# Kernel optimization log

Hardware: AMD Instinct MI355X
Metric: run time of the kernel (lower is better)

Reference implementation:

```python
import jax, jax.numpy as jnp
import numpy as np
from functools import partial

EPS = 1e-5
TAU = 0.1

def bn(x, g, b, axes):
    m = jnp.mean(x, axis=axes, keepdims=True)
    v = jnp.var(x, axis=axes, keepdims=True)
    return (x - m) * jax.lax.rsqrt(v + EPS) * g + b

def conv(x, w, b):
    # x: NCHW, w: OIHW, stride 1, padding 1
    y = jax.lax.conv_general_dilated(x, w, (1, 1), ((1, 1), (1, 1)),
                                     dimension_numbers=('NCHW', 'OIHW', 'NCHW'))
    return y + b[None, :, None, None]

def maxpool2(x):
    return jax.lax.reduce_window(x, -jnp.inf, jax.lax.max, (1, 1, 2, 2), (1, 1, 2, 2), 'VALID')

def setup_inputs() -> dict:
    key = jax.random.key(0)
    ks = jax.random.split(key, 24)
    s = 0.02
    B = 4096
    d = {}
    d['input_data'] = jax.random.normal(ks[0], (B, 3, 32, 32), jnp.float32)
    d['conv1_w'] = jax.random.normal(ks[1], (32, 3, 3, 3), jnp.float32) * s
    d['conv1_b'] = jnp.zeros((32,), jnp.float32)
    d['bn1_g'] = jnp.ones((32,), jnp.float32); d['bn1_b'] = jnp.zeros((32,), jnp.float32)
    d['conv2_w'] = jax.random.normal(ks[2], (64, 32, 3, 3), jnp.float32) * s
    d['conv2_b'] = jnp.zeros((64,), jnp.float32)
    d['bn2_g'] = jnp.ones((64,), jnp.float32); d['bn2_b'] = jnp.zeros((64,), jnp.float32)
    d['conv3_w'] = jax.random.normal(ks[3], (128, 64, 3, 3), jnp.float32) * s
    d['conv3_b'] = jnp.zeros((128,), jnp.float32)
    d['bn3_g'] = jnp.ones((128,), jnp.float32); d['bn3_b'] = jnp.zeros((128,), jnp.float32)
    d['pre_w'] = jax.random.normal(ks[4], (1024, 8192), jnp.float32) * s
    d['pre_b'] = jnp.zeros((1024,), jnp.float32)
    d['bnp_g'] = jnp.ones((1024,), jnp.float32); d['bnp_b'] = jnp.zeros((1024,), jnp.float32)
    d['disc_w'] = jax.random.normal(ks[5], (384, 1024), jnp.float32) * s
    d['disc_b'] = jnp.zeros((384,), jnp.float32)
    d['bnd_g'] = jnp.ones((384,), jnp.float32); d['bnd_b'] = jnp.zeros((384,), jnp.float32)
    d['dfc_w'] = jax.random.normal(ks[6], (2, 384), jnp.float32) * s
    d['dfc_b'] = jnp.zeros((2,), jnp.float32)
    d['sw_w'] = jax.random.normal(ks[7], (2, 384), jnp.float32) * s
    d['sw_b'] = jnp.zeros((2,), jnp.float32)
    # partitioned classifier: P=2, Linear(1024 -> 192) + ReLU + Linear(192 -> 10)
    d['p1_w'] = jax.random.normal(ks[8], (2, 192, 1024), jnp.float32) * s
    d['p1_b'] = jnp.zeros((2, 192), jnp.float32)
    d['p2_w'] = jax.random.normal(ks[9], (2, 10, 192), jnp.float32) * s
    d['p2_b'] = jnp.zeros((2, 10), jnp.float32)
    return d

def reference(input_data, conv1_w, conv1_b, bn1_g, bn1_b, conv2_w, conv2_b, bn2_g, bn2_b,
              conv3_w, conv3_b, bn3_g, bn3_b, pre_w, pre_b, bnp_g, bnp_b,
              disc_w, disc_b, bnd_g, bnd_b, dfc_w, dfc_b, sw_w, sw_b,
              p1_w, p1_b, p2_w, p2_b):
    B = input_data.shape[0]
    # feature extractor
    x = jax.nn.relu(bn(conv(input_data, conv1_w, conv1_b), bn1_g[None, :, None, None], bn1_b[None, :, None, None], (0, 2, 3)))
    x = maxpool2(x)
    x = jax.nn.relu(bn(conv(x, conv2_w, conv2_b), bn2_g[None, :, None, None], bn2_b[None, :, None, None], (0, 2, 3)))
    x = maxpool2(x)
    x = jax.nn.relu(bn(conv(x, conv3_w, conv3_b), bn3_g[None, :, None, None], bn3_b[None, :, None, None], (0, 2, 3)))
    feat = x.reshape(B, -1)  # [B, 8192]
    feat = jax.nn.relu(bn(feat @ pre_w.T + pre_b, bnp_g[None, :], bnp_b[None, :], (0,)))  # [B, 1024]
    # discriminator branch
    dpen = jax.nn.relu(bn(feat @ disc_w.T + disc_b, bnd_g[None, :], bnd_b[None, :], (0,)))  # [B, 384]
    domain_output = dpen @ dfc_w.T + dfc_b  # [B, 2]
    sw_logits = dpen @ sw_w.T + sw_b  # [B, P]
    # gumbel-softmax (soft) + multinomial sample of partition
    key = jax.random.key(42)
    k1, k2 = jax.random.split(key)
    u = jax.random.uniform(k1, sw_logits.shape, jnp.float32, 1e-10, 1.0)
    gumbel = -jnp.log(-jnp.log(u))
    y = jax.nn.softmax((sw_logits + gumbel) / TAU, axis=-1)  # [B, P]
    partition_idx = jax.random.categorical(k2, jnp.log(y + 1e-20), axis=-1)  # [B]
    # per-partition expert MLP computed densely (P=2), then gather chosen partition
    h = jax.nn.relu(jnp.einsum('bi,poi->pbo', feat, p1_w) + p1_b[:, None, :])  # [P, B, 192]
    logits = jnp.einsum('pbo,pco->pbc', h, p2_w) + p2_b[:, None, :]  # [P, B, 10]
    sel = logits[partition_idx, jnp.arange(B)]  # [B, 10]
    # original multiplies single-element stack by full gumbel vector and sums -> scale by sum(y)=1
    class_output_partitioned = sel * jnp.sum(y, axis=1, keepdims=True)
    return (class_output_partitioned, domain_output, partition_idx)
```

## Files before the change

### kernel.cpp

```cpp
#include <hip/hip_runtime.h>
#include <cstdint>
#include <cstddef>

typedef __attribute__((ext_vector_type(8))) short short8;
typedef __attribute__((ext_vector_type(4))) float f32x4;

__host__ __device__ inline void threefry2x32(uint32_t k0, uint32_t k1,
                                             uint32_t x0, uint32_t x1,
                                             uint32_t& o0, uint32_t& o1) {
  uint32_t ks2 = k0 ^ k1 ^ 0x1BD11BDAu;
  uint32_t v0 = x0 + k0, v1 = x1 + k1;
#define TF_R(r) { v0 += v1; v1 = (v1 << (r)) | (v1 >> (32 - (r))); v1 ^= v0; }
  TF_R(13) TF_R(15) TF_R(26) TF_R(6)
  v0 += k1; v1 += ks2 + 1u;
  TF_R(17) TF_R(29) TF_R(16) TF_R(24)
  v0 += ks2; v1 += k0 + 2u;
  TF_R(13) TF_R(15) TF_R(26) TF_R(6)
  v0 += k0; v1 += k1 + 3u;
  TF_R(17) TF_R(29) TF_R(16) TF_R(24)
  v0 += k1; v1 += ks2 + 4u;
  TF_R(13) TF_R(15) TF_R(26) TF_R(6)
  v0 += ks2; v1 += k0 + 5u;
#undef TF_R
  o0 = v0; o1 = v1;
}

__device__ __forceinline__ uint32_t tf_bits32(uint32_t k0, uint32_t k1, uint32_t j) {
  uint32_t o0, o1;
  threefry2x32(k0, k1, 0u, j, o0, o1);
  return o0 ^ o1;
}

__device__ __forceinline__ float u01_from_bits(uint32_t bits) {
  return __uint_as_float((bits >> 9) | 0x3f800000u) - 1.0f;
}

__device__ __forceinline__ float waveSum(float v) {
#pragma unroll
  for (int off = 32; off > 0; off >>= 1) v += __shfl_down(v, off, 64);
  return v;
}

__global__ __launch_bounds__(256) void conv1_fused_kernel(
    const float* __restrict__ in, const float* __restrict__ w,
    float* __restrict__ outraw, float* __restrict__ partials) {
  __shared__ float ins[3 * 34 * 34];
  __shared__ float red[4][64];
  const int b = blockIdx.x, t = threadIdx.x;
  for (int i = t; i < 3 * 34 * 34; i += 256) {
    int ci = i / 1156, r = i % 1156, iy = r / 34, ix = r % 34;
    int y = iy - 1, x = ix - 1;
    float v = 0.f;
    if ((unsigned)y < 32u && (unsigned)x < 32u)
      v = in[(((size_t)b * 3 + ci) * 32 + y) * 32 + x];
    ins[i] = v;
  }
  __syncthreads();
  const int py = t >> 4, px = t & 15, wv = t >> 6, ln = t & 63;
  float win[3][4][4];
#pragma unroll
  for (int ci = 0; ci < 3; ci++)
#pragma unroll
    for (int r = 0; r < 4; r++)
#pragma unroll
      for (int c = 0; c < 4; c++)
        win[ci][r][c] = ins[ci * 1156 + (2 * py + r) * 34 + (2 * px + c)];
#pragma unroll 1
  for (int co = 0; co < 32; co++) {
    float acc00 = 0.f, acc01 = 0.f, acc10 = 0.f, acc11 = 0.f;
#pragma unroll
    for (int ci = 0; ci < 3; ci++) {
      const float* wp = w + (co * 3 + ci) * 9;
#pragma unroll
      for (int dy = 0; dy < 3; dy++)
#pragma unroll
        for (int dx = 0; dx < 3; dx++) {
          float wvv = wp[dy * 3 + dx];
          acc00 += win[ci][dy][dx] * wvv;
          acc01 += win[ci][dy][dx + 1] * wvv;
          acc10 += win[ci][dy + 1][dx] * wvv;
          acc11 += win[ci][dy + 1][dx + 1] * wvv;
        }
    }
    float sm = acc00 + acc01 + acc10 + acc11;
    float sq = acc00 * acc00 + acc01 * acc01 + acc10 * acc10 + acc11 * acc11;
    float s = waveSum(sm), q = waveSum(sq);
    if (ln == 0) { red[wv][2 * co] = s; red[wv][2 * co + 1] = q; }
    float m = fmaxf(fmaxf(acc00, acc01), fmaxf(acc10, acc11));
    outraw[(((size_t)b * 32 + co) * 16 + py) * 16 + px] = m;
  }
  __syncthreads();
  for (int i = t; i < 64; i += 256)
    partials[(size_t)b * 64 + i] = red[0][i] + red[1][i] + red[2][i] + red[3][i];
}

__device__ __forceinline__ uint32_t pack_bf16q(float x) {
  uint32_t u = __float_as_uint(x);
  uint32_t hi = (u + 0x7fffu + ((u >> 16) & 1u)) & 0xffff0000u;
  float r = x - __uint_as_float(hi);
  uint32_t v = __float_as_uint(r);
  uint32_t lo = (v + 0x7fffu + ((v >> 16) & 1u)) >> 16;
  return hi | lo;
}

__global__ void cvt_bf16q_kernel(const float* X, uint32_t* Y, int n4) {
  int i = blockIdx.x * blockDim.x + threadIdx.x;
  if (i >= n4) return;
  float4 x = ((const float4*)X)[i];
  uint4 o;
  o.x = pack_bf16q(x.x); o.y = pack_bf16q(x.y);
  o.z = pack_bf16q(x.z); o.w = pack_bf16q(x.w);
  ((uint4*)Y)[i] = o;
}

__global__ void prep_w2_kernel(const float* __restrict__ w, short* __restrict__ wh,
                               short* __restrict__ wl) {
  int idx = blockIdx.x * 256 + threadIdx.x;
  if (idx >= 64 * 32 * 9) return;
  int tp = idx % 9, rem = idx / 9;
  int ci = rem % 32, co = rem / 32;
  uint32_t pq = pack_bf16q(w[idx]);
  size_t o = ((size_t)tp * 64 + co) * 32 + ci;
  wh[o] = (short)(pq >> 16);
  wl[o] = (short)(pq & 0xffffu);
}

__global__ void prep_w3_kernel(const float* __restrict__ w, short* __restrict__ wh,
                               short* __restrict__ wl) {
  int idx = blockIdx.x * 256 + threadIdx.x;
  if (idx >= 128 * 64 * 9) return;
  int tp = idx % 9, rem = idx / 9;
  int ci = rem % 64, co = rem / 64;
  uint32_t pq = pack_bf16q(w[idx]);
  size_t o = ((size_t)tp * 128 + co) * 64 + ci;
  wh[o] = (short)(pq >> 16);
  wl[o] = (short)(pq & 0xffffu);
}

__global__ __launch_bounds__(256) void conv2_mfma_kernel(
    const uint32_t* __restrict__ inq, const short* __restrict__ wh,
    const short* __restrict__ wl, float* __restrict__ outpool,
    float* __restrict__ partials) {
  __shared__ short Xh[324 * 32], Xl[324 * 32];
  __shared__ float red[4][128];
  const int b = blockIdx.x, t = threadIdx.x;
  for (int i = t; i < 324 * 16; i += 256) {
    int row = i >> 4;
    int py = row / 18, pxx = row % 18;
    if (py == 0 || py == 17 || pxx == 0 || pxx == 17) {
      ((uint32_t*)Xh)[i] = 0u;
      ((uint32_t*)Xl)[i] = 0u;
    }
  }
  for (int i = t; i < 4096; i += 256) {
    int p = i >> 8, px = i & 255;
    int y = px >> 4, x = px & 15;
    uint32_t ua = inq[((size_t)b * 32 + 2 * p) * 256 + px];
    uint32_t ub = inq[((size_t)b * 32 + 2 * p + 1) * 256 + px];
    uint32_t h = (ua >> 16) | (ub & 0xffff0000u);
    uint32_t l = (ua & 0xffffu) | (ub << 16);
    int row = (y + 1) * 18 + (x + 1);
    int ci2 = (2 * p) ^ ((row & 3) << 3);
    ((uint32_t*)Xh)[(row * 32 + ci2) >> 1] = h;
    ((uint32_t*)Xl)[(row * 32 + ci2) >> 1] = l;
  }
  __syncthreads();
  const int w = t >> 6, l = t & 63;
  const int lr = l & 15, lg = l >> 4;
  f32x4 acc[4][4];
#pragma unroll
  for (int i = 0; i < 4; i++)
#pragma unroll
    for (int j = 0; j < 4; j++) acc[i][j] = (f32x4){0.f, 0.f, 0.f, 0.f};
#pragma unroll 1
  for (int tap = 0; tap < 9; tap++) {
    const int dy = tap / 3, dx = tap % 3;
    short8 awh[4], awl[4];
#pragma unroll
    for (int i = 0; i < 4; i++) {
      size_t off = ((size_t)tap * 64 + i * 16 + lr) * 32 + lg * 8;
      awh[i] = *(const short8*)(wh + off);
      awl[i] = *(const short8*)(wl + off);
    }
    short8 bxh[4], bxl[4];
#pragma unroll
    for (int j = 0; j < 4; j++) {
      int y = w * 4 + j, x = lr;
      int row = (y + dy) * 18 + (x + dx);
      int ci = (lg * 8) ^ ((row & 3) << 3);
      bxh[j] = *(const short8*)&Xh[row * 32 + ci];
      bxl[j] = *(const short8*)&Xl[row * 32 + ci];
    }
#pragma unroll
    for (int i = 0; i < 4; i++)
#pragma unroll
      for (int j = 0; j < 4; j++) {
        acc[i][j] = __builtin_amdgcn_mfma_f32_16x16x32_bf16(awh[i], bxh[j], acc[i][j], 0, 0, 0);
        acc[i][j] = __builtin_amdgcn_mfma_f32_16x16x32_bf16(awh[i], bxl[j], acc[i][j], 0, 0, 0);
        acc[i][j] = __builtin_amdgcn_mfma_f32_16x16x32_bf16(awl[i], bxh[j], acc[i][j], 0, 0, 0);
      }
  }
#pragma unroll
  for (int i = 0; i < 4; i++)
#pragma unroll
    for (int r = 0; r < 4; r++) {
      int co = i * 16 + lg * 4 + r;
      float v0 = acc[i][0][r], v1 = acc[i][1][r], v2 = acc[i][2][r], v3 = acc[i][3][r];
      float s = v0 + v1 + v2 + v3;
      float q = v0 * v0 + v1 * v1 + v2 * v2 + v3 * v3;
#pragma unroll
      for (int off = 1; off <= 8; off <<= 1) {
        s += __shfl_xor(s, off, 64);
        q += __shfl_xor(q, off, 64);
      }
      if (lr == 0) { red[w][2 * co] = s; red[w][2 * co + 1] = q; }
      float h0 = fmaxf(v0, __shfl_xor(v0, 1, 64));
      float h1 = fmaxf(v1, __shfl_xor(v1, 1, 64));
      float h2 = fmaxf(v2, __shfl_xor(v2, 1, 64));
      float h3 = fmaxf(v3, __shfl_xor(v3, 1, 64));
      float pm0 = fmaxf(h0, h1);
      float pm1 = fmaxf(h2, h3);
      if ((lr & 1) == 0) {
        size_t base = ((size_t)b * 64 + co) * 64 + (w * 2) * 8 + (lr >> 1);
        outpool[base] = pm0;
        outpool[base + 8] = pm1;
      }
    }
  __syncthreads();
  for (int i = t; i < 128; i += 256)
    partials[(size_t)b * 128 + i] = red[0][i] + red[1][i] + red[2][i] + red[3][i];
}

__global__ __launch_bounds__(256) void conv3_mfma_kernel(
    const uint32_t* __restrict__ inq, const short* __restrict__ wh,
    const short* __restrict__ wl, float* __restrict__ outraw,
    float* __restrict__ partials) {
  __shared__ short Xh[100 * 64], Xl[100 * 64];
  __shared__ float red[256];
  const int b = blockIdx.x, t = threadIdx.x;
  for (int i = t; i < 100 * 32; i += 256) {
    int row = i >> 5;
    int py = row / 10, pxx = row % 10;
    if (py == 0 || py == 9 || pxx == 0 || pxx == 9) {
      ((uint32_t*)Xh)[i] = 0u;
      ((uint32_t*)Xl)[i] = 0u;
    }
  }
  for (int i = t; i < 2048; i += 256) {
    int p = i >> 6, px = i & 63;
    int y = px >> 3, x = px & 7;
    uint32_t ua = inq[((size_t)b * 64 + 2 * p) * 64 + px];
    uint32_t ub = inq[((size_t)b * 64 + 2 * p + 1) * 64 + px];
    uint32_t h = (ua >> 16) | (ub & 0xffff0000u);
    uint32_t l = (ua & 0xffffu) | (ub << 16);
    int row = (y + 1) * 10 + (x + 1);
    int ci2 = (2 * p) ^ ((row & 7) << 3);
    ((uint32_t*)Xh)[(row * 64 + ci2) >> 1] = h;
    ((uint32_t*)Xl)[(row * 64 + ci2) >> 1] = l;
  }
  __syncthreads();
  const int w = t >> 6, l = t & 63;
  const int lr = l & 15, lg = l >> 4;
  const int co_base = w * 32;
  f32x4 acc[2][4];
#pragma unroll
  for (int i = 0; i < 2; i++)
#pragma unroll
    for (int j = 0; j < 4; j++) acc[i][j] = (f32x4){0.f, 0.f, 0.f, 0.f};
#pragma unroll 1
  for (int tap = 0; tap < 9; tap++) {
    const int dy = tap / 3, dx = tap % 3;
#pragma unroll
    for (int sl = 0; sl < 2; sl++) {
      short8 awh[2], awl[2];
#pragma unroll
      for (int i = 0; i < 2; i++) {
        size_t off = ((size_t)tap * 128 + co_base + i * 16 + lr) * 64 + sl * 32 + lg * 8;
        awh[i] = *(const short8*)(wh + off);
        awl[i] = *(const short8*)(wl + off);
      }
      short8 bxh[4], bxl[4];
#pragma unroll
      for (int j = 0; j < 4; j++) {
        int px = j * 16 + lr;
        int row = ((px >> 3) + dy) * 10 + (px & 7) + dx;
        int ci = (sl * 32 + lg * 8) ^ ((row & 7) << 3);
        bxh[j] = *(const short8*)&Xh[row * 64 + ci];
        bxl[j] = *(const short8*)&Xl[row * 64 + ci];
      }
#pragma unroll
      for (int i = 0; i < 2; i++)
#pragma unroll
        for (int j = 0; j < 4; j++) {
          acc[i][j] = __builtin_amdgcn_mfma_f32_16x16x32_bf16(awh[i], bxh[j], acc[i][j], 0, 0, 0);
          acc[i][j] = __builtin_amdgcn_mfma_f32_16x16x32_bf16(awh[i], bxl[j], acc[i][j], 0, 0, 0);
          acc[i][j] = __builtin_amdgcn_mfma_f32_16x16x32_bf16(awl[i], bxh[j], acc[i][j], 0, 0, 0);
        }
    }
  }
#pragma unroll
  for (int i = 0; i < 2; i++)
#pragma unroll
    for (int r = 0; r < 4; r++) {
      int co = co_base + i * 16 + lg * 4 + r;
      float s = 0.f, q = 0.f;
#pragma unroll
      for (int j = 0; j < 4; j++) {
        float v = acc[i][j][r];
        outraw[((size_t)b * 128 + co) * 64 + j * 16 + lr] = v;
        s += v; q += v * v;
      }
#pragma unroll
      for (int off = 1; off <= 8; off <<= 1) {
        s += __shfl_xor(s, off, 64);
        q += __shfl_xor(q, off, 64);
      }
      if (lr == 0) { red[2 * co] = s; red[2 * co + 1] = q; }
    }
  __syncthreads();
  for (int i = t; i < 256; i += 256) partials[(size_t)b * 256 + i] = red[i];
}

__global__ __launch_bounds__(256) void reduce_partials_kernel(
    const float* __restrict__ partials, int nblk, int Q, double* __restrict__ sums) {
  int q = blockIdx.x;
  double acc = 0.0;
  for (int i = threadIdx.x; i < nblk; i += 256) acc += (double)partials[(size_t)i * Q + q];
  __shared__ double red[256];
  red[threadIdx.x] = acc;
  __syncthreads();
  for (int s = 128; s > 0; s >>= 1) {
    if (threadIdx.x < s) red[threadIdx.x] += red[threadIdx.x + s];
    __syncthreads();
  }
  if (threadIdx.x == 0) sums[q] = red[0];
}

__global__ __launch_bounds__(1024) void col_stats_kernel(
    const float* __restrict__ X, int R, int C, int nch, double* __restrict__ sums) {
  int c0 = blockIdx.x * 64, chunk = blockIdx.y;
  int cl = threadIdx.x & 63, rg = threadIdx.x >> 6;
  int rows = R / nch, rbeg = chunk * rows, rend = rbeg + rows;
  double s = 0.0, sq = 0.0;
  for (int r = rbeg + rg; r < rend; r += 16) {
    float v = X[(size_t)r * C + c0 + cl];
    s += v; sq += (double)v * (double)v;
  }
  __shared__ double red[16][64][2];
  red[rg][cl][0] = s; red[rg][cl][1] = sq;
  __syncthreads();
  if (rg == 0) {
    for (int i = 1; i < 16; i++) { s += red[i][cl][0]; sq += red[i][cl][1]; }
    sums[(size_t)chunk * 2 * C + 2 * (c0 + cl)] = s;
    sums[(size_t)chunk * 2 * C + 2 * (c0 + cl) + 1] = sq;
  }
}

__global__ void bn_finalize_kernel(const double* __restrict__ sums, int nch, int cst2,
                                   const float* __restrict__ g, const float* __restrict__ b,
                                   float* __restrict__ scale, float* __restrict__ shift,
                                   int C, double invN) {
  int c = blockIdx.x * blockDim.x + threadIdx.x;
  if (c >= C) return;
  double s = 0.0, sq = 0.0;
  for (int ch = 0; ch < nch; ch++) {
    s += sums[(size_t)ch * cst2 + 2 * c];
    sq += sums[(size_t)ch * cst2 + 2 * c + 1];
  }
  double m = s * invN;
  double v = sq * invN - m * m;
  double sc = (double)g[c] / sqrt(v + 1e-5);
  scale[c] = (float)sc;
  shift[c] = (float)((double)b[c] - m * sc);
}

template <int LOGHW, int CMASK>
__global__ void bn_relu_pack_vec4_kernel(float* __restrict__ X,
                                         const float* __restrict__ scale,
                                         const float* __restrict__ shift, int n4) {
  int i = blockIdx.x * blockDim.x + threadIdx.x;
  if (i >= n4) return;
  int c = ((i << 2) >> LOGHW) & CMASK;
  float4 v = ((float4*)X)[i];
  float sc = scale[c], sh = shift[c];
  uint4 o;
  o.x = pack_bf16q(fmaxf(v.x * sc + sh, 0.f));
  o.y = pack_bf16q(fmaxf(v.y * sc + sh, 0.f));
  o.z = pack_bf16q(fmaxf(v.z * sc + sh, 0.f));
  o.w = pack_bf16q(fmaxf(v.w * sc + sh, 0.f));
  ((uint4*)X)[i] = o;
}

__global__ void bn_relu_pack_cols4_kernel(float* __restrict__ X,
                                          const float* __restrict__ scale,
                                          const float* __restrict__ shift,
                                          int n4, int C4) {
  int i = blockIdx.x * blockDim.x + threadIdx.x;
  if (i >= n4) return;
  int c4 = i % C4;
  float4 v = ((float4*)X)[i];
  float4 sc = ((const float4*)scale)[c4];
  float4 sh = ((const float4*)shift)[c4];
  uint4 o;
  o.x = pack_bf16q(fmaxf(v.x * sc.x + sh.x, 0.f));
  o.y = pack_bf16q(fmaxf(v.y * sc.y + sh.y, 0.f));
  o.z = pack_bf16q(fmaxf(v.z * sc.z + sh.z, 0.f));
  o.w = pack_bf16q(fmaxf(v.w * sc.w + sh.w, 0.f));
  ((uint4*)X)[i] = o;
}

__global__ void bn_relu_cols4_kernel(float* __restrict__ X, const float* __restrict__ scale,
                                     const float* __restrict__ shift, int n4, int C4) {
  int i = blockIdx.x * blockDim.x + threadIdx.x;
  if (i >= n4) return;
  int c4 = i % C4;
  float4 v = ((float4*)X)[i];
  float4 sc = ((const float4*)scale)[c4];
  float4 sh = ((const float4*)shift)[c4];
  v.x = fmaxf(v.x * sc.x + sh.x, 0.f);
  v.y = fmaxf(v.y * sc.y + sh.y, 0.f);
  v.z = fmaxf(v.z * sc.z + sh.z, 0.f);
  v.w = fmaxf(v.w * sc.w + sh.w, 0.f);
  ((float4*)X)[i] = v;
}

__global__ void add_vec4_kernel(float* __restrict__ X, const float* __restrict__ Y, int n4) {
  int i = blockIdx.x * blockDim.x + threadIdx.x;
  if (i >= n4) return;
  float4 a = ((float4*)X)[i];
  float4 b = ((const float4*)Y)[i];
  a.x += b.x; a.y += b.y; a.z += b.z; a.w += b.w;
  ((float4*)X)[i] = a;
}

__device__ __forceinline__ int swz16(int row) {
  return ((row & 3) ^ ((row >> 2) & 3)) << 3;
}

template <int BIASRELU>
__global__ __launch_bounds__(256) void gemm_bf16q_kernel(
    const uint32_t* __restrict__ A, const uint32_t* __restrict__ B,
    const float* __restrict__ bias, float* __restrict__ C, int M, int N, int K) {
  __shared__ short Ah[128 * 32], Al[128 * 32], Bh[64 * 32], Bl[64 * 32];
  const int t = threadIdx.x;
  const int nTN = N >> 6;
  const int mPer = (M >> 7) >> 3;
  const int bid = blockIdx.x;
  const int xcd = bid & 7, qq = bid >> 3;
  const int m0 = (xcd * mPer + qq / nTN) << 7;
  const int n0 = (qq % nTN) << 6;
  const int w = t >> 6, l = t & 63;
  const int wrow = (w >> 1) << 6, wcol = (w & 1) << 5;
  const int lr = l & 15, lg = l >> 4;
  const int ar = t >> 1, akh = (t & 1) << 4;
  const int br = t >> 2, bkh = (t & 3) << 3;
  const int asw = swz16(ar), bsw = swz16(br);
  const uint32_t* Ap = A + (size_t)(m0 + ar) * K + akh;
  const uint32_t* Bp = B + (size_t)(n0 + br) * K + bkh;
  f32x4 acc[4][2];
#pragma unroll
  for (int i = 0; i < 4; i++)
#pragma unroll
    for (int j = 0; j < 2; j++) acc[i][j] = (f32x4){0.f, 0.f, 0.f, 0.f};
  uint4 ra0 = *(const uint4*)(Ap + 0), ra1 = *(const uint4*)(Ap + 4);
  uint4 ra2 = *(const uint4*)(Ap + 8), ra3 = *(const uint4*)(Ap + 12);
  uint4 rb0 = *(const uint4*)(Bp + 0), rb1 = *(const uint4*)(Bp + 4);
  const int NS = K >> 5;
#define STORE_G(ARR_H, ARR_L, ROW, KB, SW, U)                                   \
    {                                                                           \
      uint32_t h0 = (U.x >> 16) | (U.y & 0xffff0000u);                          \
      uint32_t h1 = (U.z >> 16) | (U.w & 0xffff0000u);                          \
      uint32_t l0 = (U.x & 0xffffu) | (U.y << 16);                              \
      uint32_t l1 = (U.z & 0xffffu) | (U.w << 16);                              \
      int idx = (ROW) * 32 + ((KB) ^ (SW));                                     \
      *(uint2*)&ARR_H[idx] = make_uint2(h0, h1);                                \
      *(uint2*)&ARR_L[idx] = make_uint2(l0, l1);                                \
    }
  for (int s = 0; s < NS; s++) {
    __syncthreads();
    STORE_G(Ah, Al, ar, akh + 0, asw, ra0)
    STORE_G(Ah, Al, ar, akh + 4, asw, ra1)
    STORE_G(Ah, Al, ar, akh + 8, asw, ra2)
    STORE_G(Ah, Al, ar, akh + 12, asw, ra3)
    STORE_G(Bh, Bl, br, bkh + 0, bsw, rb0)
    STORE_G(Bh, Bl, br, bkh + 4, bsw, rb1)
    __syncthreads();
    if (s + 1 < NS) {
      int ko = (s + 1) << 5;
      ra0 = *(const uint4*)(Ap + ko); ra1 = *(const uint4*)(Ap + ko + 4);
      ra2 = *(const uint4*)(Ap + ko + 8); ra3 = *(const uint4*)(Ap + ko + 12);
      rb0 = *(const uint4*)(Bp + ko); rb1 = *(const uint4*)(Bp + ko + 4);
    }
    short8 ahf[4], alf[4], bhf[2], blf[2];
#pragma unroll
    for (int i = 0; i < 4; i++) {
      int R = wrow + i * 16 + lr;
      int kk = (lg << 3) ^ swz16(R);
      ahf[i] = *(const short8*)&Ah[R * 32 + kk];
      alf[i] = *(const short8*)&Al[R * 32 + kk];
    }
#pragma unroll
    for (int j = 0; j < 2; j++) {
      int Cc = wcol + j * 16 + lr;
      int kk = (lg << 3) ^ swz16(Cc);
      bhf[j] = *(const short8*)&Bh[Cc * 32 + kk];
      blf[j] = *(const short8*)&Bl[Cc * 32 + kk];
    }
#pragma unroll
    for (int i = 0; i < 4; i++)
#pragma unroll
      for (int j = 0; j < 2; j++) {
        acc[i][j] = __builtin_amdgcn_mfma_f32_16x16x32_bf16(ahf[i], bhf[j], acc[i][j], 0, 0, 0);
        acc[i][j] = __builtin_amdgcn_mfma_f32_16x16x32_bf16(ahf[i], blf[j], acc[i][j], 0, 0, 0);
        acc[i][j] = __builtin_amdgcn_mfma_f32_16x16x32_bf16(alf[i], bhf[j], acc[i][j], 0, 0, 0);
      }
  }
#pragma unroll
  for (int i = 0; i < 4; i++)
#pragma unroll
    for (int j = 0; j < 2; j++) {
      int n = n0 + wcol + j * 16 + lr;
#pragma unroll
      for (int r = 0; r < 4; r++) {
        int m = m0 + wrow + i * 16 + lg * 4 + r;
        float v = acc[i][j][r];
        if (BIASRELU) v = fmaxf(v + bias[n], 0.f);
        C[(size_t)m * N + n] = v;
      }
    }
}

__global__ __launch_bounds__(256, 2) void gemm_bf16q_big_kernel(
    const uint32_t* __restrict__ A, const uint32_t* __restrict__ B,
    float* __restrict__ C0, float* __restrict__ C1, int M, int N, int K) {
  __shared__ short Ah[128 * 32], Al[128 * 32], Bh[128 * 32], Bl[128 * 32];
  const int t = threadIdx.x;
  const int nTN = N >> 7;
  const int tiles = (M >> 7) * nTN;
  const int mPer = (M >> 7) >> 3;
  const int split = blockIdx.x / tiles;
  const int bid = blockIdx.x % tiles;
  const int xcd = bid & 7, qq = bid >> 3;
  const int m0 = (xcd * mPer + qq / nTN) << 7;
  const int n0 = (qq % nTN) << 7;
  const int Kh = K >> 1;
  const int kbeg = split * Kh;
  float* Cout = split ? C1 : C0;
  const int w = t >> 6, l = t & 63;
  const int wrow = (w & 1) << 6, wcol = (w >> 1) << 6;
  const int lr = l & 15, lg = l >> 4;
  const int ar = t >> 1, akh = (t & 1) << 4;
  const int asw = swz16(ar);
  const uint32_t* Ap = A + (size_t)(m0 + ar) * K + kbeg + akh;
  const uint32_t* Bp = B + (size_t)(n0 + ar) * K + kbeg + akh;
  f32x4 acc[4][4];
#pragma unroll
  for (int i = 0; i < 4; i++)
#pragma unroll
    for (int j = 0; j < 4; j++) acc[i][j] = (f32x4){0.f, 0.f, 0.f, 0.f};
  uint4 ra0 = *(const uint4*)(Ap + 0), ra1 = *(const uint4*)(Ap + 4);
  uint4 ra2 = *(const uint4*)(Ap + 8), ra3 = *(const uint4*)(Ap + 12);
  uint4 rb0 = *(const uint4*)(Bp + 0), rb1 = *(const uint4*)(Bp + 4);
  uint4 rb2 = *(const uint4*)(Bp + 8), rb3 = *(const uint4*)(Bp + 12);
  const int NS = Kh >> 5;
  for (int s = 0; s < NS; s++) {
    __syncthreads();
    STORE_G(Ah, Al, ar, akh + 0, asw, ra0)
    STORE_G(Ah, Al, ar, akh + 4, asw, ra1)
    STORE_G(Ah, Al, ar, akh + 8, asw, ra2)
    STORE_G(Ah, Al, ar, akh + 12, asw, ra3)
    STORE_G(Bh, Bl, ar, akh + 0, asw, rb0)
    STORE_G(Bh, Bl, ar, akh + 4, asw, rb1)
    STORE_G(Bh, Bl, ar, akh + 8, asw, rb2)
    STORE_G(Bh, Bl, ar, akh + 12, asw, rb3)
    __syncthreads();
    if (s + 1 < NS) {
      int ko = (s + 1) << 5;
      ra0 = *(const uint4*)(Ap + ko); ra1 = *(const uint4*)(Ap + ko + 4);
      ra2 = *(const uint4*)(Ap + ko + 8); ra3 = *(const uint4*)(Ap + ko + 12);
      rb0 = *(const uint4*)(Bp + ko); rb1 = *(const uint4*)(Bp + ko + 4);
      rb2 = *(const uint4*)(Bp + ko + 8); rb3 = *(const uint4*)(Bp + ko + 12);
    }
    short8 ahf[4], alf[4], bhf[4], blf[4];
#pragma unroll
    for (int i = 0; i < 4; i++) {
      int R = wrow + i * 16 + lr;
      int kk = (lg << 3) ^ swz16(R);
      ahf[i] = *(const short8*)&Ah[R * 32 + kk];
      alf[i] = *(const short8*)&Al[R * 32 + kk];
    }
#pragma unroll
    for (int j = 0; j < 4; j++) {
      int Cc = wcol + j * 16 + lr;
      int kk = (lg << 3) ^ swz16(Cc);
      bhf[j] = *(const short8*)&Bh[Cc * 32 + kk];
      blf[j] = *(const short8*)&Bl[Cc * 32 + kk];
    }
#pragma unroll
    for (int i = 0; i < 4; i++)
#pragma unroll
      for (int j = 0; j < 4; j++) {
        acc[i][j] = __builtin_amdgcn_mfma_f32_16x16x32_bf16(ahf[i], bhf[j], acc[i][j], 0, 0, 0);
        acc[i][j] = __builtin_amdgcn_mfma_f32_16x16x32_bf16(ahf[i], blf[j], acc[i][j], 0, 0, 0);
        acc[i][j] = __builtin_amdgcn_mfma_f32_16x16x32_bf16(alf[i], bhf[j], acc[i][j], 0, 0, 0);
      }
  }
#undef STORE_G
#pragma unroll
  for (int i = 0; i < 4; i++)
#pragma unroll
    for (int j = 0; j < 4; j++) {
      int n = n0 + wcol + j * 16 + lr;
#pragma unroll
      for (int r = 0; r < 4; r++) {
        int m = m0 + wrow + i * 16 + lg * 4 + r;
        Cout[(size_t)m * N + n] = acc[i][j][r];
      }
    }
}

__global__ __launch_bounds__(256) void heads_kernel(
    const float* __restrict__ dpen, const float* __restrict__ dfc_w,
    const float* __restrict__ dfc_b, const float* __restrict__ sw_w,
    const float* __restrict__ sw_b, float* __restrict__ out_dom,
    float* __restrict__ swbuf) {
  int t = blockIdx.x * 256 + threadIdx.x;
  int b = t >> 2, j = t & 3;
  const float* row = dpen + (size_t)b * 384;
  const float* wr = (j < 2) ? (dfc_w + j * 384) : (sw_w + (j - 2) * 384);
  double s = 0.0;
  for (int k = 0; k < 384; k++) s += (double)row[k] * (double)wr[k];
  s += (double)((j < 2) ? dfc_b[j] : sw_b[j - 2]);
  if (j < 2) out_dom[b * 2 + j] = (float)s;
  else swbuf[b * 2 + (j - 2)] = (float)s;
}

__global__ __launch_bounds__(256) void partition_kernel(
    const float* __restrict__ swbuf, float* __restrict__ out_pid,
    int* __restrict__ pidxI, float* __restrict__ ysum,
    uint32_t k1a, uint32_t k1b, uint32_t k2a, uint32_t k2b) {
  int b = blockIdx.x * 256 + threadIdx.x;
  if (b >= 4096) return;
  uint32_t j0 = (uint32_t)(2 * b), j1 = (uint32_t)(2 * b + 1);
  float f0 = u01_from_bits(tf_bits32(k1a, k1b, j0));
  float f1 = u01_from_bits(tf_bits32(k1a, k1b, j1));
  const float MINV = 1e-10f;
  float u0 = fmaxf(MINV, f0 * (1.0f - MINV) + MINV);
  float u1 = fmaxf(MINV, f1 * (1.0f - MINV) + MINV);
  double g0 = -log(-log((double)u0));
  double g1 = -log(-log((double)u1));
  double s0 = (double)swbuf[2 * b], s1 = (double)swbuf[2 * b + 1];
  double x0 = (s0 + g0) / 0.1;
  double x1 = (s1 + g1) / 0.1;
  double mx = fmax(x0, x1);
  double e0 = exp(x0 - mx), e1 = exp(x1 - mx);
  double es = e0 + e1;
  double y0 = e0 / es, y1 = e1 / es;
  float h0 = u01_from_bits(tf_bits32(k2a, k2b, j0));
  float h1 = u01_from_bits(tf_bits32(k2a, k2b, j1));
  const float TINY = 1.17549435e-38f;
  float v0 = fmaxf(TINY, h0 * (1.0f - TINY) + TINY);
  float v1 = fmaxf(TINY, h1 * (1.0f - TINY) + TINY);
  double gg0 = -log(-log((double)v0));
  double gg1 = -log(-log((double)v1));
  double l0 = log(y0 + 1e-20) + gg0;
  double l1 = log(y1 + 1e-20) + gg1;
  int p = (l1 > l0) ? 1 : 0;
  out_pid[b] = (float)p;
  pidxI[b] = p;
  ysum[b] = (float)(y0 + y1);
}

__global__ __launch_bounds__(256) void final_kernel(
    const float* __restrict__ h, const float* __restrict__ p2w,
    const float* __restrict__ p2b, const int* __restrict__ pidxI,
    const float* __restrict__ ysum, float* __restrict__ out0) {
  int t = blockIdx.x * 256 + threadIdx.x;
  if (t >= 40960) return;
  int b = t / 10, c = t % 10;
  int p = pidxI[b];
  const float* hr = h + (size_t)b * 384 + p * 192;
  const float* wr = p2w + ((size_t)p * 10 + c) * 192;
  float s = 0.f;
  for (int o = 0; o < 192; o++) s += hr[o] * wr[o];
  s += p2b[p * 10 + c];
  out0[t] = s * ysum[b];
}

extern "C" void kernel_launch(void* const* d_in, const int* in_sizes, int n_in,
                              void* d_out, int out_size, void* d_ws, size_t ws_size,
                              hipStream_t stream) {
  const float* input   = (const float*)d_in[0];
  const float* conv1_w = (const float*)d_in[1];
  const float* bn1_g   = (const float*)d_in[3];
  const float* bn1_b   = (const float*)d_in[4];
  const float* conv2_w = (const float*)d_in[5];
  const float* bn2_g   = (const float*)d_in[7];
  const float* bn2_b   = (const float*)d_in[8];
  const float* conv3_w = (const float*)d_in[9];
  const float* bn3_g   = (const float*)d_in[11];
  const float* bn3_b   = (const float*)d_in[12];
  const float* pre_w   = (const float*)d_in[13];
  const float* bnp_g   = (const float*)d_in[15];
  const float* bnp_b   = (const float*)d_in[16];
  const float* disc_w  = (const float*)d_in[17];
  const float* bnd_g   = (const float*)d_in[19];
  const float* bnd_b   = (const float*)d_in[20];
  const float* dfc_w   = (const float*)d_in[21];
  const float* dfc_b   = (const float*)d_in[22];
  const float* sw_w    = (const float*)d_in[23];
  const float* sw_b    = (const float*)d_in[24];
  const float* p1_w    = (const float*)d_in[25];
  const float* p1_b    = (const float*)d_in[26];
  const float* p2_w    = (const float*)d_in[27];
  const float* p2_b    = (const float*)d_in[28];

  float* W = (float*)d_ws;
  float* pool1  = W + 0;
  uint32_t* pool1q = (uint32_t*)pool1;
  float* pool2  = W + 33554432;
  uint32_t* pool2q = (uint32_t*)pool2;
  float* act3   = W + 0;
  uint32_t* Acvt = (uint32_t*)(W + 0);
  uint32_t* Bcvt = (uint32_t*)(W + 33554432);
  uint32_t* discq = (uint32_t*)(W + 41943040);
  uint32_t* p1q   = (uint32_t*)(W + 42336256);
  float* csplit = W + 42729472;
  float* featp  = W + 50331648;
  uint32_t* featq = (uint32_t*)featp;
  short* wh3    = (short*)(W + 50331648);
  short* wl3    = (short*)(W + 50368512);
  short* wh2    = (short*)(W + 50405376);
  short* wl2    = (short*)(W + 50414592);
  float* dpen   = W + 54525952;
  float* hbuf   = W + 56098816;
  float* swbuf  = W + 57671680;
  float* ysum   = W + 57679872;
  int*   pidxI  = (int*)(W + 57683968);
  float* part   = W + 57688064;
  double* sums  = (double*)(W + 58736640);
  float* scale  = W + 58769408;
  float* shift  = W + 58770432;

  float* out_cls = (float*)d_out;
  float* out_dom = out_cls + 40960;
  float* out_pid = out_cls + 49152;

  uint32_t k1a, k1b, k2a, k2b;
  threefry2x32(0u, 42u, 0u, 0u, k1a, k1b);
  threefry2x32(0u, 42u, 0u, 1u, k2a, k2b);

  conv1_fused_kernel<<<dim3(4096), dim3(256), 0, stream>>>(input, conv1_w, pool1, part);
  reduce_partials_kernel<<<dim3(64), dim3(256), 0, stream>>>(part, 4096, 64, sums);
  bn_finalize_kernel<<<dim3(1), dim3(64), 0, stream>>>(sums, 1, 0, bn1_g, bn1_b, scale, shift, 32, 1.0 / (4096.0 * 1024.0));
  bn_relu_pack_vec4_kernel<8, 31><<<dim3(32768), dim3(256), 0, stream>>>(pool1, scale, shift, 8388608);

  prep_w2_kernel<<<dim3(72), dim3(256), 0, stream>>>(conv2_w, wh2, wl2);
  conv2_mfma_kernel<<<dim3(4096), dim3(256), 0, stream>>>(pool1q, wh2, wl2, pool2, part);
  reduce_partials_kernel<<<dim3(128), dim3(256), 0, stream>>>(part, 4096, 128, sums);
  bn_finalize_kernel<<<dim3(1), dim3(64), 0, stream>>>(sums, 1, 0, bn2_g, bn2_b, scale, shift, 64, 1.0 / (4096.0 * 256.0));
  bn_relu_pack_vec4_kernel<6, 63><<<dim3(16384), dim3(256), 0, stream>>>(pool2, scale, shift, 4194304);

  prep_w3_kernel<<<dim3(288), dim3(256), 0, stream>>>(conv3_w, wh3, wl3);
  conv3_mfma_kernel<<<dim3(4096), dim3(256), 0, stream>>>(pool2q, wh3, wl3, act3, part);
  reduce_partials_kernel<<<dim3(256), dim3(256), 0, stream>>>(part, 4096, 256, sums);
  bn_finalize_kernel<<<dim3(1), dim3(128), 0, stream>>>(sums, 1, 0, bn3_g, bn3_b, scale, shift, 128, 1.0 / (4096.0 * 64.0));
  bn_relu_pack_vec4_kernel<6, 127><<<dim3(32768), dim3(256), 0, stream>>>(act3, scale, shift, 8388608);

  cvt_bf16q_kernel<<<dim3(8192), dim3(256), 0, stream>>>(pre_w, Bcvt, 2097152);
  gemm_bf16q_big_kernel<<<dim3(512), dim3(256), 0, stream>>>(Acvt, Bcvt, featp, csplit, 4096, 1024, 8192);
  add_vec4_kernel<<<dim3(4096), dim3(256), 0, stream>>>(featp, csplit, 1048576);
  col_stats_kernel<<<dim3(16, 8), dim3(1024), 0, stream>>>(featp, 4096, 1024, 8, sums);
  bn_finalize_kernel<<<dim3(4), dim3(256), 0, stream>>>(sums, 8, 2048, bnp_g, bnp_b, scale, shift, 1024, 1.0 / 4096.0);
  bn_relu_pack_cols4_kernel<<<dim3(4096), dim3(256), 0, stream>>>(featp, scale, shift, 1048576, 256);

  cvt_bf16q_kernel<<<dim3(384), dim3(256), 0, stream>>>(disc_w, discq, 98304);
  cvt_bf16q_kernel<<<dim3(384), dim3(256), 0, stream>>>(p1_w, p1q, 98304);
  gemm_bf16q_kernel<0><<<dim3(192), dim3(256), 0, stream>>>(featq, discq, (const float*)nullptr, dpen, 4096, 384, 1024);
  col_stats_kernel<<<dim3(6, 8), dim3(1024), 0, stream>>>(dpen, 4096, 384, 8, sums);
  bn_finalize_kernel<<<dim3(2), dim3(256), 0, stream>>>(sums, 8, 768, bnd_g, bnd_b, scale, shift, 384, 1.0 / 4096.0);
  bn_relu_cols4_kernel<<<dim3(1536), dim3(256), 0, stream>>>(dpen, scale, shift, 393216, 96);

  heads_kernel<<<dim3(64), dim3(256), 0, stream>>>(dpen, dfc_w, dfc_b, sw_w, sw_b, out_dom, swbuf);
  partition_kernel<<<dim3(16), dim3(256), 0, stream>>>(swbuf, out_pid, pidxI, ysum, k1a, k1b, k2a, k2b);

  gemm_bf16q_kernel<1><<<dim3(192), dim3(256), 0, stream>>>(featq, p1q, p1_b, hbuf, 4096, 384, 1024);
  final_kernel<<<dim3(160), dim3(256), 0, stream>>>(hbuf, p2_w, p2_b, pidxI, ysum, out_cls);
}
```

Before: 927.6 us.

## Fuse BN+ReLU+pack into consumer conv/GEMM loads and parallelize heads

Removes the standalone BN-ReLU-pack passes after conv1, conv2 and conv3. Each consumer (conv2, conv3, the big GEMM) now reads raw fp32 activations, applies the per-channel scale/shift and ReLU, and packs to split bf16 on the fly. The split-K add kernel is folded into col_stats and the final BN pack, and the heads kernel is rewritten to use one wavefront per row with shuffle reductions. This saves several full read/write passes over large activation buffers. In exchange the GEMM and conv loads double in width (fp32 instead of packed) and the GEMM recomputes the conversion per tile.

```diff
diff --git a/kernel.cpp b/kernel.cpp
--- a/kernel.cpp
+++ b/kernel.cpp
@@ -103,6 +103,15 @@
   return hi | lo;
 }
 
+__device__ __forceinline__ uint4 pk4bn(float4 v, float sc, float sh) {
+  uint4 o;
+  o.x = pack_bf16q(fmaxf(v.x * sc + sh, 0.f));
+  o.y = pack_bf16q(fmaxf(v.y * sc + sh, 0.f));
+  o.z = pack_bf16q(fmaxf(v.z * sc + sh, 0.f));
+  o.w = pack_bf16q(fmaxf(v.w * sc + sh, 0.f));
+  return o;
+}
+
 __global__ void cvt_bf16q_kernel(const float* X, uint32_t* Y, int n4) {
   int i = blockIdx.x * blockDim.x + threadIdx.x;
   if (i >= n4) return;
@@ -138,7 +147,8 @@
 }
 
 __global__ __launch_bounds__(256) void conv2_mfma_kernel(
-    const uint32_t* __restrict__ inq, const short* __restrict__ wh,
+    const float* __restrict__ in, const float* __restrict__ scale1,
+    const float* __restrict__ shift1, const short* __restrict__ wh,
     const short* __restrict__ wl, float* __restrict__ outpool,
     float* __restrict__ partials) {
   __shared__ short Xh[324 * 32], Xl[324 * 32];
@@ -155,8 +165,11 @@
   for (int i = t; i < 4096; i += 256) {
     int p = i >> 8, px = i & 255;
     int y = px >> 4, x = px & 15;
-    uint32_t ua = inq[((size_t)b * 32 + 2 * p) * 256 + px];
-    uint32_t ub = inq[((size_t)b * 32 + 2 * p + 1) * 256 + px];
+    float va = in[((size_t)b * 32 + 2 * p) * 256 + px];
+    float vb = in[((size_t)b * 32 + 2 * p + 1) * 256 + px];
+    va = fmaxf(va * scale1[2 * p] + shift1[2 * p], 0.f);
+    vb = fmaxf(vb * scale1[2 * p + 1] + shift1[2 * p + 1], 0.f);
+    uint32_t ua = pack_bf16q(va), ub = pack_bf16q(vb);
     uint32_t h = (ua >> 16) | (ub & 0xffff0000u);
     uint32_t l = (ua & 0xffffu) | (ub << 16);
     int row = (y + 1) * 18 + (x + 1);
@@ -232,7 +245,8 @@
 }
 
 __global__ __launch_bounds__(256) void conv3_mfma_kernel(
-    const uint32_t* __restrict__ inq, const short* __restrict__ wh,
+    const float* __restrict__ in, const float* __restrict__ scale2,
+    const float* __restrict__ shift2, const short* __restrict__ wh,
     const short* __restrict__ wl, float* __restrict__ outraw,
     float* __restrict__ partials) {
   __shared__ short Xh[100 * 64], Xl[100 * 64];
@@ -249,8 +263,11 @@
   for (int i = t; i < 2048; i += 256) {
     int p = i >> 6, px = i & 63;
     int y = px >> 3, x = px & 7;
-    uint32_t ua = inq[((size_t)b * 64 + 2 * p) * 64 + px];
-    uint32_t ub = inq[((size_t)b * 64 + 2 * p + 1) * 64 + px];
+    float va = in[((size_t)b * 64 + 2 * p) * 64 + px];
+    float vb = in[((size_t)b * 64 + 2 * p + 1) * 64 + px];
+    va = fmaxf(va * scale2[2 * p] + shift2[2 * p], 0.f);
+    vb = fmaxf(vb * scale2[2 * p + 1] + shift2[2 * p + 1], 0.f);
+    uint32_t ua = pack_bf16q(va), ub = pack_bf16q(vb);
     uint32_t h = (ua >> 16) | (ub & 0xffff0000u);
     uint32_t l = (ua & 0xffffu) | (ub << 16);
     int row = (y + 1) * 10 + (x + 1);
@@ -337,13 +354,16 @@
 }
 
 __global__ __launch_bounds__(1024) void col_stats_kernel(
-    const float* __restrict__ X, int R, int C, int nch, double* __restrict__ sums) {
+    const float* __restrict__ X, const float* __restrict__ Y,
+    int R, int C, int nch, double* __restrict__ sums) {
   int c0 = blockIdx.x * 64, chunk = blockIdx.y;
   int cl = threadIdx.x & 63, rg = threadIdx.x >> 6;
   int rows = R / nch, rbeg = chunk * rows, rend = rbeg + rows;
   double s = 0.0, sq = 0.0;
   for (int r = rbeg + rg; r < rend; r += 16) {
-    float v = X[(size_t)r * C + c0 + cl];
+    size_t idx = (size_t)r * C + c0 + cl;
+    float v = X[idx];
+    if (Y) v += Y[idx];
     s += v; sq += (double)v * (double)v;
   }
   __shared__ double red[16][64][2];
@@ -374,24 +394,8 @@
   shift[c] = (float)((double)b[c] - m * sc);
 }
 
-template <int LOGHW, int CMASK>
-__global__ void bn_relu_pack_vec4_kernel(float* __restrict__ X,
-                                         const float* __restrict__ scale,
-                                         const float* __restrict__ shift, int n4) {
-  int i = blockIdx.x * blockDim.x + threadIdx.x;
-  if (i >= n4) return;
-  int c = ((i << 2) >> LOGHW) & CMASK;
-  float4 v = ((float4*)X)[i];
-  float sc = scale[c], sh = shift[c];
-  uint4 o;
-  o.x = pack_bf16q(fmaxf(v.x * sc + sh, 0.f));
-  o.y = pack_bf16q(fmaxf(v.y * sc + sh, 0.f));
-  o.z = pack_bf16q(fmaxf(v.z * sc + sh, 0.f));
-  o.w = pack_bf16q(fmaxf(v.w * sc + sh, 0.f));
-  ((uint4*)X)[i] = o;
-}
-
 __global__ void bn_relu_pack_cols4_kernel(float* __restrict__ X,
+                                          const float* __restrict__ Y,
                                           const float* __restrict__ scale,
                                           const float* __restrict__ shift,
                                           int n4, int C4) {
@@ -399,6 +403,10 @@
   if (i >= n4) return;
   int c4 = i % C4;
   float4 v = ((float4*)X)[i];
+  if (Y) {
+    float4 y = ((const float4*)Y)[i];
+    v.x += y.x; v.y += y.y; v.z += y.z; v.w += y.w;
+  }
   float4 sc = ((const float4*)scale)[c4];
   float4 sh = ((const float4*)shift)[c4];
   uint4 o;
@@ -422,15 +430,6 @@
   v.z = fmaxf(v.z * sc.z + sh.z, 0.f);
   v.w = fmaxf(v.w * sc.w + sh.w, 0.f);
   ((float4*)X)[i] = v;
-}
-
-__global__ void add_vec4_kernel(float* __restrict__ X, const float* __restrict__ Y, int n4) {
-  int i = blockIdx.x * blockDim.x + threadIdx.x;
-  if (i >= n4) return;
-  float4 a = ((float4*)X)[i];
-  float4 b = ((const float4*)Y)[i];
-  a.x += b.x; a.y += b.y; a.z += b.z; a.w += b.w;
-  ((float4*)X)[i] = a;
 }
 
 __device__ __forceinline__ int swz16(int row) {
@@ -531,7 +530,8 @@
 }
 
 __global__ __launch_bounds__(256, 2) void gemm_bf16q_big_kernel(
-    const uint32_t* __restrict__ A, const uint32_t* __restrict__ B,
+    const float* __restrict__ A, const uint32_t* __restrict__ B,
+    const float* __restrict__ scale, const float* __restrict__ shift,
     float* __restrict__ C0, float* __restrict__ C1, int M, int N, int K) {
   __shared__ short Ah[128 * 32], Al[128 * 32], Bh[128 * 32], Bl[128 * 32];
   const int t = threadIdx.x;
@@ -551,24 +551,28 @@
   const int lr = l & 15, lg = l >> 4;
   const int ar = t >> 1, akh = (t & 1) << 4;
   const int asw = swz16(ar);
-  const uint32_t* Ap = A + (size_t)(m0 + ar) * K + kbeg + akh;
+  const float* Ap = A + (size_t)(m0 + ar) * K + kbeg + akh;
   const uint32_t* Bp = B + (size_t)(n0 + ar) * K + kbeg + akh;
   f32x4 acc[4][4];
 #pragma unroll
   for (int i = 0; i < 4; i++)
 #pragma unroll
     for (int j = 0; j < 4; j++) acc[i][j] = (f32x4){0.f, 0.f, 0.f, 0.f};
-  uint4 ra0 = *(const uint4*)(Ap + 0), ra1 = *(const uint4*)(Ap + 4);
-  uint4 ra2 = *(const uint4*)(Ap + 8), ra3 = *(const uint4*)(Ap + 12);
+  float4 fa0 = *(const float4*)(Ap + 0), fa1 = *(const float4*)(Ap + 4);
+  float4 fa2 = *(const float4*)(Ap + 8), fa3 = *(const float4*)(Ap + 12);
   uint4 rb0 = *(const uint4*)(Bp + 0), rb1 = *(const uint4*)(Bp + 4);
   uint4 rb2 = *(const uint4*)(Bp + 8), rb3 = *(const uint4*)(Bp + 12);
   const int NS = Kh >> 5;
   for (int s = 0; s < NS; s++) {
+    int ch = (kbeg + akh + (s << 5)) >> 6;
+    float sc = scale[ch], sh = shift[ch];
+    uint4 ua0 = pk4bn(fa0, sc, sh), ua1 = pk4bn(fa1, sc, sh);
+    uint4 ua2 = pk4bn(fa2, sc, sh), ua3 = pk4bn(fa3, sc, sh);
     __syncthreads();
-    STORE_G(Ah, Al, ar, akh + 0, asw, ra0)
-    STORE_G(Ah, Al, ar, akh + 4, asw, ra1)
-    STORE_G(Ah, Al, ar, akh + 8, asw, ra2)
-    STORE_G(Ah, Al, ar, akh + 12, asw, ra3)
+    STORE_G(Ah, Al, ar, akh + 0, asw, ua0)
+    STORE_G(Ah, Al, ar, akh + 4, asw, ua1)
+    STORE_G(Ah, Al, ar, akh + 8, asw, ua2)
+    STORE_G(Ah, Al, ar, akh + 12, asw, ua3)
     STORE_G(Bh, Bl, ar, akh + 0, asw, rb0)
     STORE_G(Bh, Bl, ar, akh + 4, asw, rb1)
     STORE_G(Bh, Bl, ar, akh + 8, asw, rb2)
@@ -576,8 +580,8 @@
     __syncthreads();
     if (s + 1 < NS) {
       int ko = (s + 1) << 5;
-      ra0 = *(const uint4*)(Ap + ko); ra1 = *(const uint4*)(Ap + ko + 4);
-      ra2 = *(const uint4*)(Ap + ko + 8); ra3 = *(const uint4*)(Ap + ko + 12);
+      fa0 = *(const float4*)(Ap + ko); fa1 = *(const float4*)(Ap + ko + 4);
+      fa2 = *(const float4*)(Ap + ko + 8); fa3 = *(const float4*)(Ap + ko + 12);
       rb0 = *(const uint4*)(Bp + ko); rb1 = *(const uint4*)(Bp + ko + 4);
       rb2 = *(const uint4*)(Bp + ko + 8); rb3 = *(const uint4*)(Bp + ko + 12);
     }
@@ -624,15 +628,30 @@
     const float* __restrict__ dfc_b, const float* __restrict__ sw_w,
     const float* __restrict__ sw_b, float* __restrict__ out_dom,
     float* __restrict__ swbuf) {
-  int t = blockIdx.x * 256 + threadIdx.x;
-  int b = t >> 2, j = t & 3;
+  int wv = threadIdx.x >> 6, ln = threadIdx.x & 63;
+  int b = blockIdx.x * 4 + wv;
   const float* row = dpen + (size_t)b * 384;
-  const float* wr = (j < 2) ? (dfc_w + j * 384) : (sw_w + (j - 2) * 384);
-  double s = 0.0;
-  for (int k = 0; k < 384; k++) s += (double)row[k] * (double)wr[k];
-  s += (double)((j < 2) ? dfc_b[j] : sw_b[j - 2]);
-  if (j < 2) out_dom[b * 2 + j] = (float)s;
-  else swbuf[b * 2 + (j - 2)] = (float)s;
+  double a0 = 0.0, a1 = 0.0, a2 = 0.0, a3 = 0.0;
+  for (int k = ln; k < 384; k += 64) {
+    double rv = (double)row[k];
+    a0 += rv * (double)dfc_w[k];
+    a1 += rv * (double)dfc_w[384 + k];
+    a2 += rv * (double)sw_w[k];
+    a3 += rv * (double)sw_w[384 + k];
+  }
+#pragma unroll
+  for (int off = 32; off > 0; off >>= 1) {
+    a0 += __shfl_down(a0, off, 64);
+    a1 += __shfl_down(a1, off, 64);
+    a2 += __shfl_down(a2, off, 64);
+    a3 += __shfl_down(a3, off, 64);
+  }
+  if (ln == 0) {
+    out_dom[b * 2 + 0] = (float)(a0 + (double)dfc_b[0]);
+    out_dom[b * 2 + 1] = (float)(a1 + (double)dfc_b[1]);
+    swbuf[b * 2 + 0] = (float)(a2 + (double)sw_b[0]);
+    swbuf[b * 2 + 1] = (float)(a3 + (double)sw_b[1]);
+  }
 }
 
 __global__ __launch_bounds__(256) void partition_kernel(
@@ -717,11 +736,8 @@
 
   float* W = (float*)d_ws;
   float* pool1  = W + 0;
-  uint32_t* pool1q = (uint32_t*)pool1;
   float* pool2  = W + 33554432;
-  uint32_t* pool2q = (uint32_t*)pool2;
   float* act3   = W + 0;
-  uint32_t* Acvt = (uint32_t*)(W + 0);
   uint32_t* Bcvt = (uint32_t*)(W + 33554432);
   uint32_t* discq = (uint32_t*)(W + 41943040);
   uint32_t* p1q   = (uint32_t*)(W + 42336256);
@@ -753,35 +769,31 @@
   conv1_fused_kernel<<<dim3(4096), dim3(256), 0, stream>>>(input, conv1_w, pool1, part);
   reduce_partials_kernel<<<dim3(64), dim3(256), 0, stream>>>(part, 4096, 64, sums);
   bn_finalize_kernel<<<dim3(1), dim3(64), 0, stream>>>(sums, 1, 0, bn1_g, bn1_b, scale, shift, 32, 1.0 / (4096.0 * 1024.0));
-  bn_relu_pack_vec4_kernel<8, 31><<<dim3(32768), dim3(256), 0, stream>>>(pool1, scale, shift, 8388608);
 
   prep_w2_kernel<<<dim3(72), dim3(256), 0, stream>>>(conv2_w, wh2, wl2);
-  conv2_mfma_kernel<<<dim3(4096), dim3(256), 0, stream>>>(pool1q, wh2, wl2, pool2, part);
+  conv2_mfma_kernel<<<dim3(4096), dim3(256), 0, stream>>>(pool1, scale, shift, wh2, wl2, pool2, part);
   reduce_partials_kernel<<<dim3(128), dim3(256), 0, stream>>>(part, 4096, 128, sums);
   bn_finalize_kernel<<<dim3(1), dim3(64), 0, stream>>>(sums, 1, 0, bn2_g, bn2_b, scale, shift, 64, 1.0 / (4096.0 * 256.0));
-  bn_relu_pack_vec4_kernel<6, 63><<<dim3(16384), dim3(256), 0, stream>>>(pool2, scale, shift, 4194304);
 
   prep_w3_kernel<<<dim3(288), dim3(256), 0, stream>>>(conv3_w, wh3, wl3);
-  conv3_mfma_kernel<<<dim3(4096), dim3(256), 0, stream>>>(pool2q, wh3, wl3, act3, part);
+  conv3_mfma_kernel<<<dim3(4096), dim3(256), 0, stream>>>(pool2, scale, shift, wh3, wl3, act3, part);
   reduce_partials_kernel<<<dim3(256), dim3(256), 0, stream>>>(part, 4096, 256, sums);
   bn_finalize_kernel<<<dim3(1), dim3(128), 0, stream>>>(sums, 1, 0, bn3_g, bn3_b, scale, shift, 128, 1.0 / (4096.0 * 64.0));
-  bn_relu_pack_vec4_kernel<6, 127><<<dim3(32768), dim3(256), 0, stream>>>(act3, scale, shift, 8388608);
 
   cvt_bf16q_kernel<<<dim3(8192), dim3(256), 0, stream>>>(pre_w, Bcvt, 2097152);
-  gemm_bf16q_big_kernel<<<dim3(512), dim3(256), 0, stream>>>(Acvt, Bcvt, featp, csplit, 4096, 1024, 8192);
-  add_vec4_kernel<<<dim3(4096), dim3(256), 0, stream>>>(featp, csplit, 1048576);
-  col_stats_kernel<<<dim3(16, 8), dim3(1024), 0, stream>>>(featp, 4096, 1024, 8, sums);
+  gemm_bf16q_big_kernel<<<dim3(512), dim3(256), 0, stream>>>(act3, Bcvt, scale, shift, featp, csplit, 4096, 1024, 8192);
+  col_stats_kernel<<<dim3(16, 8), dim3(1024), 0, stream>>>(featp, csplit, 4096, 1024, 8, sums);
   bn_finalize_kernel<<<dim3(4), dim3(256), 0, stream>>>(sums, 8, 2048, bnp_g, bnp_b, scale, shift, 1024, 1.0 / 4096.0);
-  bn_relu_pack_cols4_kernel<<<dim3(4096), dim3(256), 0, stream>>>(featp, scale, shift, 1048576, 256);
+  bn_relu_pack_cols4_kernel<<<dim3(4096), dim3(256), 0, stream>>>(featp, csplit, scale, shift, 1048576, 256);
 
   cvt_bf16q_kernel<<<dim3(384), dim3(256), 0, stream>>>(disc_w, discq, 98304);
   cvt_bf16q_kernel<<<dim3(384), dim3(256), 0, stream>>>(p1_w, p1q, 98304);
   gemm_bf16q_kernel<0><<<dim3(192), dim3(256), 0, stream>>>(featq, discq, (const float*)nullptr, dpen, 4096, 384, 1024);
-  col_stats_kernel<<<dim3(6, 8), dim3(1024), 0, stream>>>(dpen, 4096, 384, 8, sums);
+  col_stats_kernel<<<dim3(6, 8), dim3(1024), 0, stream>>>(dpen, (const float*)nullptr, 4096, 384, 8, sums);
   bn_finalize_kernel<<<dim3(2), dim3(256), 0, stream>>>(sums, 8, 768, bnd_g, bnd_b, scale, shift, 384, 1.0 / 4096.0);
   bn_relu_cols4_kernel<<<dim3(1536), dim3(256), 0, stream>>>(dpen, scale, shift, 393216, 96);
 
-  heads_kernel<<<dim3(64), dim3(256), 0, stream>>>(dpen, dfc_w, dfc_b, sw_w, sw_b, out_dom, swbuf);
+  heads_kernel<<<dim3(1024), dim3(256), 0, stream>>>(dpen, dfc_w, dfc_b, sw_w, sw_b, out_dom, swbuf);
   partition_kernel<<<dim3(16), dim3(256), 0, stream>>>(swbuf, out_pid, pidxI, ysum, k1a, k1b, k2a, k2b);
 
   gemm_bf16q_kernel<1><<<dim3(192), dim3(256), 0, stream>>>(featq, p1q, p1_b, hbuf, 4096, 384, 1024);
```

Result: faster. 870.5 us (-6.1%).
